# Kernel tuning notes

Hardware: AMD Instinct MI355X
Metric: run time of the kernel (lower is better)

## Reference

```python
import jax, jax.numpy as jnp
import numpy as np

B, S, L, D = 4, 8, 350, 768  # paragraphs, sentences/paragraph, padded pair length, hidden
P = B * S * (S - 1)          # number of ordered sentence pairs = 224

# pair p -> (z, j, k): same enumeration order as the torch nested loops
_IDX = np.array([(z, j, k) for z in range(B) for j in range(S) for k in range(S) if j != k])
# each pair contributes its first-sentence embedding to segment (z,j) and second to (z,k)
_SEG = np.stack([_IDX[:, 0] * S + _IDX[:, 1], _IDX[:, 0] * S + _IDX[:, 2]], axis=1).reshape(-1)  # [2P]


def setup_inputs() -> dict:
    key = jax.random.key(0)
    ks = jax.random.split(key, 8)
    sc = 0.02
    all_output = jax.random.normal(ks[0], (P, L, D), dtype=jnp.float32)
    first_sep = jax.random.randint(ks[1], (P,), 5, 150).astype(jnp.int32)           # > 1
    second_sep = (first_sep + jax.random.randint(ks[2], (P,), 5, 150)).astype(jnp.int32)  # > first_sep+1, < L
    W1 = jax.random.normal(ks[3], (D, D), dtype=jnp.float32) * sc
    b1 = jnp.zeros((D,), jnp.float32)
    v1 = jax.random.normal(ks[4], (D,), dtype=jnp.float32) * sc
    vb1 = jnp.zeros((), jnp.float32)
    W2 = jax.random.normal(ks[5], (D, D), dtype=jnp.float32) * sc
    b2 = jnp.zeros((D,), jnp.float32)
    v2 = jax.random.normal(ks[6], (D,), dtype=jnp.float32) * sc
    vb2 = jnp.zeros((), jnp.float32)
    return {"all_output": all_output, "first_sep": first_sep, "second_sep": second_sep,
            "W1": W1, "b1": b1, "v1": v1, "vb1": vb1,
            "W2": W2, "b2": b2, "v2": v2, "vb2": vb2}


def reference(all_output, first_sep, second_sep, W1, b1, v1, vb1, W2, b2, v2, vb2):
    # pair_embeddings = [CLS] token of every pair
    pair_embeddings = all_output[:, 0, :]  # [P, D]

    # ---- level one: masked attention pooling over word positions ----
    u = jnp.tanh(all_output @ W1 + b1)          # [P, L, D]
    scores = u @ v1 + vb1                       # [P, L]
    pos = jnp.arange(L)[None, :]                # [1, L]
    mask1 = (pos >= 1) & (pos < first_sep[:, None])                 # tokens 1..first_sep-1
    mask2 = (pos > first_sep[:, None]) & (pos < second_sep[:, None])  # first_sep+1..second_sep-1

    def pool(mask):
        s = jnp.where(mask, scores, -jnp.inf)
        w = jax.nn.softmax(s, axis=1)           # [P, L]
        return jnp.einsum('pl,pld->pd', w, all_output)

    e1 = pool(mask1)                            # [P, D] first-sentence embeddings
    e2 = pool(mask2)                            # [P, D] second-sentence embeddings
    emb = jnp.stack([e1, e2], axis=1).reshape(2 * P, D)  # [2P, D]

    # ---- level two: segment attention pooling per (paragraph, sentence) group ----
    seg = jnp.asarray(_SEG)                     # [2P] segment ids, num_segments = B*S
    u2 = jnp.tanh(emb @ W2 + b2)                # [2P, D]
    sc = u2 @ v2 + vb2                          # [2P]
    num_seg = B * S
    smax = jax.ops.segment_max(sc, seg, num_segments=num_seg)
    ex = jnp.exp(sc - smax[seg])
    denom = jax.ops.segment_sum(ex, seg, num_segments=num_seg)
    w = ex / denom[seg]                         # segment softmax weights
    out2 = jax.ops.segment_sum(w[:, None] * emb, seg, num_segments=num_seg).reshape(B, S, D)
    return (pair_embeddings, out2)
```

## Files before the change

kernel.cpp:

```cpp
#include <hip/hip_runtime.h>
#include <math.h>

#define LSEQ   350
#define DDIM   768
#define NPAIR  224
#define MROWS1 78400
#define NSLAB1 613

typedef short bf16x8 __attribute__((ext_vector_type(8)));
typedef float f32x4  __attribute__((ext_vector_type(4)));

typedef const unsigned int __attribute__((address_space(1)))* gas_ptr;
typedef unsigned int __attribute__((address_space(3)))* las_ptr;

__device__ __forceinline__ void gload_lds16(const void* g, void* l) {
  __builtin_amdgcn_global_load_lds((gas_ptr)g, (las_ptr)l, 16, 0, 0);
}

__device__ __forceinline__ unsigned short f2bf(float x) {
  unsigned int u = __float_as_uint(x);
  unsigned int r = (u + 0x7FFFu + ((u >> 16) & 1u)) >> 16;
  return (unsigned short)r;
}

__device__ __forceinline__ float tanh_fast(float x) {
  float e = __expf(2.f * x);
  return 1.f - 2.f / (e + 1.f);
}

__global__ __launch_bounds__(256) void k_w1t(const float* __restrict__ W,
                                             unsigned short* __restrict__ Wt) {
  __shared__ float tile[32][33];
  int bk = blockIdx.x * 32, bn = blockIdx.y * 32;
  int tx = threadIdx.x & 31, ty = threadIdx.x >> 5;
#pragma unroll
  for (int i = 0; i < 32; i += 8)
    tile[ty + i][tx] = W[(size_t)(bk + ty + i) * DDIM + bn + tx];
  __syncthreads();
#pragma unroll
  for (int i = 0; i < 32; i += 8)
    Wt[(size_t)(bn + ty + i) * DDIM + bk + tx] = f2bf(tile[tx][ty + i]);
}

__global__ __launch_bounds__(256) void k_conv(const float* __restrict__ X,
                                              const int* __restrict__ ssep,
                                              unsigned short* __restrict__ Xbf) {
  const int p = blockIdx.x, tile = blockIdx.y, z = blockIdx.z;
  if (tile * 128 >= ssep[p]) return;
  const int t = threadIdx.x;
  const size_t base4 = ((size_t)p * LSEQ + tile * 128 + z * 32) * (DDIM / 4);
  const size_t limit4 = (size_t)MROWS1 * (DDIM / 4);
  const float4* X4 = (const float4*)X;
  uint2* O2 = (uint2*)Xbf;
#pragma unroll
  for (int k = 0; k < 24; ++k) {
    size_t i4 = base4 + (size_t)k * 256 + t;
    if (i4 >= limit4) break;
    float4 x = X4[i4];
    unsigned int ux = __float_as_uint(x.x) + 0x8000u;
    unsigned int uy = __float_as_uint(x.y) + 0x8000u;
    unsigned int uz = __float_as_uint(x.z) + 0x8000u;
    unsigned int uw = __float_as_uint(x.w) + 0x8000u;
    O2[i4] = make_uint2(__builtin_amdgcn_perm(uy, ux, 0x07060302u),
                        __builtin_amdgcn_perm(uw, uz, 0x07060302u));
  }
}

__global__ __launch_bounds__(256, 4) void k_gemm_bf16(
    const unsigned short* __restrict__ Xbf, const unsigned short* __restrict__ Wt,
    const float* __restrict__ bias, const float* __restrict__ vv,
    const int* __restrict__ ssep, float* __restrict__ outs) {
  const int b = blockIdx.x;
  const int g = b / 48, r = b - g * 48;
  const int unit = g * 8 + (r & 7);
  const int nchunk = r >> 3;
  const int pair = unit / 3, tile = unit - pair * 3;
  if (tile * 128 >= ssep[pair]) return;

  const size_t arow0 = (size_t)pair * LSEQ + tile * 128;
  const int n0 = nchunk * 128;

  __shared__ unsigned short As[128 * 32];
  __shared__ unsigned short Bs[128 * 32];

  const int t = threadIdx.x;
  const int lane = t & 63, w = t >> 6;
  const int l15 = t & 15;
  const int quad = (t >> 4) & 3;
  const int wm = w >> 1, wn = w & 1;
  const int lrow = lane >> 2;
  const int lcol = (lane & 3) * 8;

  f32x4 acc[4][4];
#pragma unroll
  for (int mi = 0; mi < 4; ++mi)
#pragma unroll
    for (int ni = 0; ni < 4; ++ni)
#pragma unroll
      for (int q = 0; q < 4; ++q) acc[mi][ni][q] = 0.f;

  for (int k0 = 0; k0 < DDIM; k0 += 32) {
#pragma unroll
    for (int j = 0; j < 2; ++j) {
      int seg = w * 2 + j;
      gload_lds16(Xbf + (arow0 + seg * 16 + lrow) * DDIM + k0 + lcol, As + seg * 512);
      gload_lds16(Wt + (size_t)(n0 + seg * 16 + lrow) * DDIM + k0 + lcol, Bs + seg * 512);
    }
    __syncthreads();

    bf16x8 a[4], bfr[4];
#pragma unroll
    for (int mi = 0; mi < 4; ++mi)
      a[mi] = *(const bf16x8*)&As[(wm * 64 + mi * 16 + l15) * 32 + quad * 8];
#pragma unroll
    for (int ni = 0; ni < 4; ++ni)
      bfr[ni] = *(const bf16x8*)&Bs[(wn * 64 + ni * 16 + l15) * 32 + quad * 8];
#pragma unroll
    for (int mi = 0; mi < 4; ++mi)
#pragma unroll
      for (int ni = 0; ni < 4; ++ni)
        acc[mi][ni] = __builtin_amdgcn_mfma_f32_16x16x32_bf16(a[mi], bfr[ni], acc[mi][ni], 0, 0, 0);
    __syncthreads();
  }

  float vvv[4], bbv[4];
#pragma unroll
  for (int ni = 0; ni < 4; ++ni) {
    int n = n0 + wn * 64 + ni * 16 + l15;
    vvv[ni] = vv[n];
    bbv[ni] = bias[n];
  }
#pragma unroll
  for (int mi = 0; mi < 4; ++mi) {
#pragma unroll
    for (int reg = 0; reg < 4; ++reg) {
      float s = 0.f;
#pragma unroll
      for (int ni = 0; ni < 4; ++ni)
        s += tanh_fast(acc[mi][ni][reg] + bbv[ni]) * vvv[ni];
      s += __shfl_xor(s, 1);
      s += __shfl_xor(s, 2);
      s += __shfl_xor(s, 4);
      s += __shfl_xor(s, 8);
      if (l15 == mi * 4 + reg) {
        int l = tile * 128 + wm * 64 + mi * 16 + quad * 4 + reg;
        if (l < LSEQ) atomicAdd(&outs[pair * LSEQ + l], s);
      }
    }
  }
}

__global__ __launch_bounds__(256, 2) void k_gemm_score(
    const float* __restrict__ X, const unsigned short* __restrict__ Wt,
    const float* __restrict__ bias, const float* __restrict__ vv,
    float* __restrict__ outs, int Mrows, int swz) {
  int slab, nchunk;
  if (swz) {
    int b = blockIdx.x;
    int g = b / 48, r = b - g * 48;
    slab = g * 8 + (r & 7);
    nchunk = r >> 3;
    if (slab >= NSLAB1) return;
  } else {
    slab = blockIdx.y;
    nchunk = blockIdx.x;
  }
  const int row0 = slab * 128;
  const int n0 = nchunk * 128;

  __shared__ unsigned short As[128][40];
  __shared__ unsigned short Bs[128][40];

  const int t = threadIdx.x;
  const int l15 = t & 15;
  const int quad = (t >> 4) & 3;
  const int w = t >> 6;
  const int wm = w >> 1, wn = w & 1;
  const int ar = t >> 3;
  const int ac = (t & 7) * 4;
  const int br = t >> 2;
  const int bc = (t & 3) * 8;

  f32x4 acc[4][4];
#pragma unroll
  for (int mi = 0; mi < 4; ++mi)
#pragma unroll
    for (int ni = 0; ni < 4; ++ni)
#pragma unroll
      for (int q = 0; q < 4; ++q) acc[mi][ni][q] = 0.f;

  for (int k0 = 0; k0 < DDIM; k0 += 32) {
#pragma unroll
    for (int pass = 0; pass < 4; ++pass) {
      int rr = ar + pass * 32;
      int row = row0 + rr;
      float4 x = make_float4(0.f, 0.f, 0.f, 0.f);
      if (row < Mrows) x = *(const float4*)(X + (size_t)row * DDIM + k0 + ac);
      unsigned int ux = __float_as_uint(x.x) + 0x8000u;
      unsigned int uy = __float_as_uint(x.y) + 0x8000u;
      unsigned int uz = __float_as_uint(x.z) + 0x8000u;
      unsigned int uw = __float_as_uint(x.w) + 0x8000u;
      *(uint2*)&As[rr][ac] = make_uint2(__builtin_amdgcn_perm(uy, ux, 0x07060302u),
                                        __builtin_amdgcn_perm(uw, uz, 0x07060302u));
    }
#pragma unroll
    for (int pp = 0; pp < 2; ++pp) {
      int rr = br + pp * 64;
      *(uint4*)&Bs[rr][bc] = *(const uint4*)(Wt + (size_t)(n0 + rr) * DDIM + k0 + bc);
    }
    __syncthreads();

    bf16x8 a[4], bfr[4];
#pragma unroll
    for (int mi = 0; mi < 4; ++mi)
      a[mi] = *(const bf16x8*)&As[wm * 64 + mi * 16 + l15][quad * 8];
#pragma unroll
    for (int ni = 0; ni < 4; ++ni)
      bfr[ni] = *(const bf16x8*)&Bs[wn * 64 + ni * 16 + l15][quad * 8];
#pragma unroll
    for (int mi = 0; mi < 4; ++mi)
#pragma unroll
      for (int ni = 0; ni < 4; ++ni)
        acc[mi][ni] = __builtin_amdgcn_mfma_f32_16x16x32_bf16(a[mi], bfr[ni], acc[mi][ni], 0, 0, 0);
    __syncthreads();
  }

  float vvv[4], bbv[4];
#pragma unroll
  for (int ni = 0; ni < 4; ++ni) {
    int n = n0 + wn * 64 + ni * 16 + l15;
    vvv[ni] = vv[n];
    bbv[ni] = bias[n];
  }
#pragma unroll
  for (int mi = 0; mi < 4; ++mi) {
#pragma unroll
    for (int reg = 0; reg < 4; ++reg) {
      float s = 0.f;
#pragma unroll
      for (int ni = 0; ni < 4; ++ni)
        s += tanh_fast(acc[mi][ni][reg] + bbv[ni]) * vvv[ni];
      s += __shfl_xor(s, 1);
      s += __shfl_xor(s, 2);
      s += __shfl_xor(s, 4);
      s += __shfl_xor(s, 8);
      if (l15 == mi * 4 + reg) {
        int row = row0 + wm * 64 + mi * 16 + quad * 4 + reg;
        if (row < Mrows) atomicAdd(&outs[row], s);
      }
    }
  }
}

__device__ __forceinline__ float block_reduce(float v, bool is_max, float* redbuf) {
#pragma unroll
  for (int off = 1; off < 64; off <<= 1) {
    float o = __shfl_xor(v, off);
    v = is_max ? fmaxf(v, o) : (v + o);
  }
  int wv = threadIdx.x >> 6;
  if ((threadIdx.x & 63) == 0) redbuf[wv] = v;
  __syncthreads();
  float r = is_max ? fmaxf(fmaxf(redbuf[0], redbuf[1]), fmaxf(redbuf[2], redbuf[3]))
                   : (redbuf[0] + redbuf[1] + redbuf[2] + redbuf[3]);
  __syncthreads();
  return r;
}

__global__ __launch_bounds__(256) void k_smax(
    const float* __restrict__ scores, const int* __restrict__ fsep,
    const int* __restrict__ ssep, float* __restrict__ w1n, float* __restrict__ w2n) {
  const int p = blockIdx.x, t = threadIdx.x;
  const int fs = fsep[p], ss = ssep[p];
  __shared__ float redbuf[4];
  float s1a[2], s2a[2];
  float m1p = -INFINITY, m2p = -INFINITY;
#pragma unroll
  for (int i = 0; i < 2; ++i) {
    int l = t + i * 256;
    float s1 = -INFINITY, s2 = -INFINITY;
    if (l < LSEQ) {
      float s = scores[p * LSEQ + l];
      s1 = (l >= 1 && l < fs) ? s : -INFINITY;
      s2 = (l > fs && l < ss) ? s : -INFINITY;
    }
    s1a[i] = s1; s2a[i] = s2;
    m1p = fmaxf(m1p, s1); m2p = fmaxf(m2p, s2);
  }
  float m1 = block_reduce(m1p, true, redbuf);
  float m2 = block_reduce(m2p, true, redbuf);
  float d1p = 0.f, d2p = 0.f;
#pragma unroll
  for (int i = 0; i < 2; ++i) {
    s1a[i] = __expf(s1a[i] - m1);
    s2a[i] = __expf(s2a[i] - m2);
    d1p += s1a[i]; d2p += s2a[i];
  }
  float inv1 = 1.f / block_reduce(d1p, false, redbuf);
  float inv2 = 1.f / block_reduce(d2p, false, redbuf);
#pragma unroll
  for (int i = 0; i < 2; ++i) {
    int l = t + i * 256;
    if (l < LSEQ) {
      w1n[p * LSEQ + l] = s1a[i] * inv1;
      w2n[p * LSEQ + l] = s2a[i] * inv2;
    }
  }
}

__global__ __launch_bounds__(192) void k_pool_bf(
    const unsigned short* __restrict__ Xbf, const float* __restrict__ X,
    const float* __restrict__ w1n, const float* __restrict__ w2n,
    const int* __restrict__ ssep, float* __restrict__ emb, float* __restrict__ out) {
  const int p = blockIdx.x, c = blockIdx.y, t = threadIdx.x;
  const int ss = ssep[p];
  const size_t prow = (size_t)p * LSEQ;
  float A1[4] = {0.f, 0.f, 0.f, 0.f}, A2[4] = {0.f, 0.f, 0.f, 0.f};
  for (int l = 1 + c; l < ss; l += 8) {
    float wa = w1n[prow + l], wb = w2n[prow + l];
    uint2 xv = *(const uint2*)(Xbf + (prow + l) * DDIM + t * 4);
    float x0 = __uint_as_float((xv.x & 0xFFFFu) << 16);
    float x1 = __uint_as_float(xv.x & 0xFFFF0000u);
    float x2 = __uint_as_float((xv.y & 0xFFFFu) << 16);
    float x3 = __uint_as_float(xv.y & 0xFFFF0000u);
    A1[0] += wa * x0; A1[1] += wa * x1; A1[2] += wa * x2; A1[3] += wa * x3;
    A2[0] += wb * x0; A2[1] += wb * x1; A2[2] += wb * x2; A2[3] += wb * x3;
  }
  float* e1 = emb + (size_t)(2 * p) * DDIM + t * 4;
  float* e2 = emb + (size_t)(2 * p + 1) * DDIM + t * 4;
#pragma unroll
  for (int i = 0; i < 4; ++i) atomicAdd(&e1[i], A1[i]);
#pragma unroll
  for (int i = 0; i < 4; ++i) atomicAdd(&e2[i], A2[i]);
  if (c == 0) {
    *(float4*)(out + (size_t)p * DDIM + t * 4) = *(const float4*)(X + prow * DDIM + t * 4);
  }
}

__global__ __launch_bounds__(256) void k_pool(
    const float* __restrict__ X, const float* __restrict__ scores,
    const int* __restrict__ fsep, const int* __restrict__ ssep,
    float* __restrict__ emb, float* __restrict__ out) {
  const int p = blockIdx.x;
  const int c = blockIdx.y;
  const int t = threadIdx.x;
  const int fs = fsep[p], ss = ssep[p];
  __shared__ float sw1[LSEQ], sw2[LSEQ];
  __shared__ float redbuf[4];

  float m1p = -INFINITY, m2p = -INFINITY;
  for (int l = t; l < LSEQ; l += 256) {
    float s = scores[p * LSEQ + l];
    float s1 = (l >= 1 && l < fs) ? s : -INFINITY;
    float s2 = (l > fs && l < ss) ? s : -INFINITY;
    sw1[l] = s1; sw2[l] = s2;
    m1p = fmaxf(m1p, s1); m2p = fmaxf(m2p, s2);
  }
  __syncthreads();
  float m1 = block_reduce(m1p, true, redbuf);
  float m2 = block_reduce(m2p, true, redbuf);
  float d1p = 0.f, d2p = 0.f;
  for (int l = t; l < LSEQ; l += 256) {
    float e1v = __expf(sw1[l] - m1);
    float e2v = __expf(sw2[l] - m2);
    sw1[l] = e1v; sw2[l] = e2v;
    d1p += e1v; d2p += e2v;
  }
  __syncthreads();
  float inv1 = 1.f / block_reduce(d1p, false, redbuf);
  float inv2 = 1.f / block_reduce(d2p, false, redbuf);
  const float* base = X + (size_t)p * LSEQ * DDIM;
  if (c == 0) {
    float* po = out + (size_t)p * DDIM;
    po[t] = base[t]; po[t + 256] = base[t + 256]; po[t + 512] = base[t + 512];
  }
  if (t < 192) {
    float4 A1 = make_float4(0.f, 0.f, 0.f, 0.f);
    float4 A2 = make_float4(0.f, 0.f, 0.f, 0.f);
    for (int l = 1 + c; l < ss; l += 8) {
      float wa = sw1[l] * inv1, wb = sw2[l] * inv2;
      float4 x = *(const float4*)(base + (size_t)l * DDIM + 4 * t);
      A1.x += wa * x.x; A1.y += wa * x.y; A1.z += wa * x.z; A1.w += wa * x.w;
      A2.x += wb * x.x; A2.y += wb * x.y; A2.z += wb * x.z; A2.w += wb * x.w;
    }
    float* e1 = emb + (size_t)(2 * p) * DDIM + 4 * t;
    float* e2 = emb + (size_t)(2 * p + 1) * DDIM + 4 * t;
    atomicAdd(&e1[0], A1.x); atomicAdd(&e1[1], A1.y);
    atomicAdd(&e1[2], A1.z); atomicAdd(&e1[3], A1.w);
    atomicAdd(&e2[0], A2.x); atomicAdd(&e2[1], A2.y);
    atomicAdd(&e2[2], A2.z); atomicAdd(&e2[3], A2.w);
  }
}

__global__ __launch_bounds__(256) void k_segout(
    const float* __restrict__ emb, const float* __restrict__ sc,
    float* __restrict__ out2) {
  const int g = blockIdx.x;
  const int z = g >> 3, j = g & 7;
  const int t = threadIdx.x;
  int ee[14];
#pragma unroll
  for (int i = 0; i < 7; ++i) ee[i] = 2 * (z * 56 + j * 7 + i);
#pragma unroll
  for (int i = 0; i < 7; ++i) {
    int j2 = i + (i >= j ? 1 : 0);
    int kk = j - (j > j2 ? 1 : 0);
    ee[7 + i] = 2 * (z * 56 + j2 * 7 + kk) + 1;
  }
  float sv[14];
  float m = -INFINITY;
#pragma unroll
  for (int i = 0; i < 14; ++i) { sv[i] = sc[ee[i]]; m = fmaxf(m, sv[i]); }
  float den = 0.f;
#pragma unroll
  for (int i = 0; i < 14; ++i) { sv[i] = __expf(sv[i] - m); den += sv[i]; }
  float inv = 1.f / den;
  float a0 = 0.f, a1 = 0.f, a2 = 0.f;
#pragma unroll
  for (int i = 0; i < 14; ++i) {
    float wgt = sv[i] * inv;
    const float* er = emb + (size_t)ee[i] * DDIM;
    a0 += wgt * er[t]; a1 += wgt * er[t + 256]; a2 += wgt * er[t + 512];
  }
  out2[(size_t)g * DDIM + t] = a0;
  out2[(size_t)g * DDIM + t + 256] = a1;
  out2[(size_t)g * DDIM + t + 512] = a2;
}

extern "C" void kernel_launch(void* const* d_in, const int* in_sizes, int n_in,
                              void* d_out, int out_size, void* d_ws, size_t ws_size,
                              hipStream_t stream) {
  const float* X  = (const float*)d_in[0];
  const int* fs   = (const int*)d_in[1];
  const int* ss   = (const int*)d_in[2];
  const float* W1 = (const float*)d_in[3];
  const float* b1 = (const float*)d_in[4];
  const float* v1 = (const float*)d_in[5];
  const float* W2 = (const float*)d_in[7];
  const float* b2 = (const float*)d_in[8];
  const float* v2 = (const float*)d_in[9];
  float* out = (float*)d_out;

  char* ws = (char*)d_ws;
  const size_t XBF_BYTES = (size_t)78464 * DDIM * 2;
  const size_t OFF_WT  = XBF_BYTES;
  const size_t OFF_SC  = OFF_WT + 1179648;
  const size_t OFF_EMB = OFF_SC + 313600;
  const size_t OFF_W1N = OFF_EMB + 1376256;
  const size_t OFF_W2N = OFF_W1N + 313600;
  const size_t NEED    = OFF_W2N + 313600;

  if (ws_size >= NEED) {
    unsigned short* Xbf = (unsigned short*)ws;
    unsigned short* Wt  = (unsigned short*)(ws + OFF_WT);
    float* scores = (float*)(ws + OFF_SC);
    float* emb    = (float*)(ws + OFF_EMB);
    float* w1n    = (float*)(ws + OFF_W1N);
    float* w2n    = (float*)(ws + OFF_W2N);
    float* sc     = scores;

    k_w1t<<<dim3(24, 24), 256, 0, stream>>>(W1, Wt);
    hipMemsetAsync(scores, 0, MROWS1 * sizeof(float), stream);
    hipMemsetAsync(emb, 0, 448 * DDIM * sizeof(float), stream);
    k_conv<<<dim3(NPAIR, 3, 4), 256, 0, stream>>>(X, ss, Xbf);
    k_gemm_bf16<<<84 * 48, 256, 0, stream>>>(Xbf, Wt, b1, v1, ss, scores);
    k_smax<<<NPAIR, 256, 0, stream>>>(scores, fs, ss, w1n, w2n);
    k_pool_bf<<<dim3(NPAIR, 8), 192, 0, stream>>>(Xbf, X, w1n, w2n, ss, emb, out);
    k_w1t<<<dim3(24, 24), 256, 0, stream>>>(W2, Wt);
    hipMemsetAsync(sc, 0, 448 * sizeof(float), stream);
    k_gemm_score<<<dim3(6, 4), 256, 0, stream>>>(emb, Wt, b2, v2, sc, 448, 0);
    k_segout<<<32, 256, 0, stream>>>(emb, sc, out + (size_t)NPAIR * DDIM);
  } else {
    unsigned short* Wt = (unsigned short*)ws;
    float* scores = (float*)(ws + 1179648);
    float* emb    = (float*)(ws + 1493248);
    float* sc     = scores;

    k_w1t<<<dim3(24, 24), 256, 0, stream>>>(W1, Wt);
    hipMemsetAsync(scores, 0, MROWS1 * sizeof(float), stream);
    hipMemsetAsync(emb, 0, 448 * DDIM * sizeof(float), stream);
    k_gemm_score<<<77 * 48, 256, 0, stream>>>(X, Wt, b1, v1, scores, MROWS1, 1);
    k_pool<<<dim3(NPAIR, 8), 256, 0, stream>>>(X, scores, fs, ss, emb, out);
    k_w1t<<<dim3(24, 24), 256, 0, stream>>>(W2, Wt);
    hipMemsetAsync(sc, 0, 448 * sizeof(float), stream);
    k_gemm_score<<<dim3(6, 4), 256, 0, stream>>>(emb, Wt, b2, v2, sc, 448, 0);
    k_segout<<<32, 256, 0, stream>>>(emb, sc, out + (size_t)NPAIR * DDIM);
  }
}
```

Measured before the change: 546.7 us.

## Compact valid token rows across pairs before bf16 GEMM and fuse softmax into pooling

A prefix scan over second_sep computes per-pair row offsets. Only the valid rows 1..ss-1 are converted to bf16 into one contiguous buffer, with a rowmap back to the original positions. The level-one GEMM then tiles this compacted buffer in dense 128-row slabs, so it no longer wastes work on padded per-pair tiles. The softmax and pooling kernels are merged, both weight transposes run in one launch, and the memsets are combined. The cost is extra indirection and an atomic scatter through rowmap. The grid is fixed at 65*48 blocks, which assumes the compacted rows fit in 520 slabs.

```diff
diff --git a/kernel.cpp b/kernel.cpp
--- a/kernel.cpp
+++ b/kernel.cpp
@@ -6,6 +6,7 @@
 #define NPAIR  224
 #define MROWS1 78400
 #define NSLAB1 613
+#define MAXSLAB 520
 
 typedef short bf16x8 __attribute__((ext_vector_type(8)));
 typedef float f32x4  __attribute__((ext_vector_type(4)));
@@ -26,6 +27,42 @@
 __device__ __forceinline__ float tanh_fast(float x) {
   float e = __expf(2.f * x);
   return 1.f - 2.f / (e + 1.f);
+}
+
+__global__ __launch_bounds__(256) void k_scan(const int* __restrict__ ssep,
+                                              int* __restrict__ off) {
+  __shared__ int buf[256];
+  const int t = threadIdx.x;
+  int v = (t < NPAIR) ? (ssep[t] - 1) : 0;
+  buf[t] = v;
+  __syncthreads();
+#pragma unroll
+  for (int d = 1; d < 256; d <<= 1) {
+    int add = (t >= d) ? buf[t - d] : 0;
+    __syncthreads();
+    buf[t] += add;
+    __syncthreads();
+  }
+  if (t < NPAIR) off[t] = buf[t] - v;
+  if (t == NPAIR - 1) off[NPAIR] = buf[t];
+}
+
+__global__ __launch_bounds__(256) void k_wt2(const float* __restrict__ W1,
+                                             const float* __restrict__ W2,
+                                             unsigned short* __restrict__ Wt1,
+                                             unsigned short* __restrict__ Wt2) {
+  const float* W = blockIdx.z ? W2 : W1;
+  unsigned short* Wt = blockIdx.z ? Wt2 : Wt1;
+  __shared__ float tile[32][33];
+  int bk = blockIdx.x * 32, bn = blockIdx.y * 32;
+  int tx = threadIdx.x & 31, ty = threadIdx.x >> 5;
+#pragma unroll
+  for (int i = 0; i < 32; i += 8)
+    tile[ty + i][tx] = W[(size_t)(bk + ty + i) * DDIM + bn + tx];
+  __syncthreads();
+#pragma unroll
+  for (int i = 0; i < 32; i += 8)
+    Wt[(size_t)(bn + ty + i) * DDIM + bk + tx] = f2bf(tile[tx][ty + i]);
 }
 
 __global__ __launch_bounds__(256) void k_w1t(const float* __restrict__ W,
@@ -44,40 +81,47 @@
 
 __global__ __launch_bounds__(256) void k_conv(const float* __restrict__ X,
                                               const int* __restrict__ ssep,
-                                              unsigned short* __restrict__ Xbf) {
+                                              const int* __restrict__ off,
+                                              unsigned short* __restrict__ Xbf,
+                                              int* __restrict__ rowmap) {
   const int p = blockIdx.x, tile = blockIdx.y, z = blockIdx.z;
-  if (tile * 128 >= ssep[p]) return;
+  const int nrow = ssep[p] - 1;
+  const int r0 = tile * 128 + z * 32;
+  if (r0 >= nrow) return;
   const int t = threadIdx.x;
-  const size_t base4 = ((size_t)p * LSEQ + tile * 128 + z * 32) * (DDIM / 4);
-  const size_t limit4 = (size_t)MROWS1 * (DDIM / 4);
-  const float4* X4 = (const float4*)X;
-  uint2* O2 = (uint2*)Xbf;
-#pragma unroll
-  for (int k = 0; k < 24; ++k) {
-    size_t i4 = base4 + (size_t)k * 256 + t;
-    if (i4 >= limit4) break;
-    float4 x = X4[i4];
-    unsigned int ux = __float_as_uint(x.x) + 0x8000u;
-    unsigned int uy = __float_as_uint(x.y) + 0x8000u;
-    unsigned int uz = __float_as_uint(x.z) + 0x8000u;
-    unsigned int uw = __float_as_uint(x.w) + 0x8000u;
-    O2[i4] = make_uint2(__builtin_amdgcn_perm(uy, ux, 0x07060302u),
-                        __builtin_amdgcn_perm(uw, uz, 0x07060302u));
-  }
-}
-
-__global__ __launch_bounds__(256, 4) void k_gemm_bf16(
+  const int o = off[p];
+  if (t < 192) {
+    for (int i = 0; i < 32; ++i) {
+      int r = r0 + i;
+      if (r >= nrow) break;
+      float4 x = *(const float4*)(X + ((size_t)p * LSEQ + 1 + r) * DDIM + t * 4);
+      unsigned int ux = __float_as_uint(x.x) + 0x8000u;
+      unsigned int uy = __float_as_uint(x.y) + 0x8000u;
+      unsigned int uz = __float_as_uint(x.z) + 0x8000u;
+      unsigned int uw = __float_as_uint(x.w) + 0x8000u;
+      *(uint2*)(Xbf + (size_t)(o + r) * DDIM + t * 4) =
+          make_uint2(__builtin_amdgcn_perm(uy, ux, 0x07060302u),
+                     __builtin_amdgcn_perm(uw, uz, 0x07060302u));
+    }
+  } else if (t < 224) {
+    int r = r0 + (t - 192);
+    if (r < nrow) rowmap[o + r] = p * LSEQ + 1 + r;
+  }
+}
+
+__global__ __launch_bounds__(256, 4) void k_gemm_c(
     const unsigned short* __restrict__ Xbf, const unsigned short* __restrict__ Wt,
     const float* __restrict__ bias, const float* __restrict__ vv,
-    const int* __restrict__ ssep, float* __restrict__ outs) {
+    const int* __restrict__ off, const int* __restrict__ rowmap,
+    float* __restrict__ scores) {
+  const int Mtotal = off[NPAIR];
   const int b = blockIdx.x;
   const int g = b / 48, r = b - g * 48;
-  const int unit = g * 8 + (r & 7);
+  const int slab = g * 8 + (r & 7);
   const int nchunk = r >> 3;
-  const int pair = unit / 3, tile = unit - pair * 3;
-  if (tile * 128 >= ssep[pair]) return;
-
-  const size_t arow0 = (size_t)pair * LSEQ + tile * 128;
+  if (slab * 128 >= Mtotal) return;
+
+  const size_t arow0 = (size_t)slab * 128;
   const int n0 = nchunk * 128;
 
   __shared__ unsigned short As[128 * 32];
@@ -143,8 +187,8 @@
       s += __shfl_xor(s, 4);
       s += __shfl_xor(s, 8);
       if (l15 == mi * 4 + reg) {
-        int l = tile * 128 + wm * 64 + mi * 16 + quad * 4 + reg;
-        if (l < LSEQ) atomicAdd(&outs[pair * LSEQ + l], s);
+        int row = (int)arow0 + wm * 64 + mi * 16 + quad * 4 + reg;
+        if (row < Mtotal) atomicAdd(&scores[rowmap[row]], s);
       }
     }
   }
@@ -267,73 +311,62 @@
   return r;
 }
 
-__global__ __launch_bounds__(256) void k_smax(
+__global__ __launch_bounds__(256) void k_pool2(
+    const unsigned short* __restrict__ Xbf, const float* __restrict__ X,
     const float* __restrict__ scores, const int* __restrict__ fsep,
-    const int* __restrict__ ssep, float* __restrict__ w1n, float* __restrict__ w2n) {
-  const int p = blockIdx.x, t = threadIdx.x;
+    const int* __restrict__ ssep, const int* __restrict__ off,
+    float* __restrict__ emb, float* __restrict__ out) {
+  const int p = blockIdx.x, c = blockIdx.y, t = threadIdx.x;
   const int fs = fsep[p], ss = ssep[p];
+  __shared__ float sw1[LSEQ], sw2[LSEQ];
   __shared__ float redbuf[4];
-  float s1a[2], s2a[2];
+
   float m1p = -INFINITY, m2p = -INFINITY;
-#pragma unroll
-  for (int i = 0; i < 2; ++i) {
-    int l = t + i * 256;
-    float s1 = -INFINITY, s2 = -INFINITY;
-    if (l < LSEQ) {
-      float s = scores[p * LSEQ + l];
-      s1 = (l >= 1 && l < fs) ? s : -INFINITY;
-      s2 = (l > fs && l < ss) ? s : -INFINITY;
-    }
-    s1a[i] = s1; s2a[i] = s2;
+  for (int l = t; l < LSEQ; l += 256) {
+    float s = scores[p * LSEQ + l];
+    float s1 = (l >= 1 && l < fs) ? s : -INFINITY;
+    float s2 = (l > fs && l < ss) ? s : -INFINITY;
+    sw1[l] = s1; sw2[l] = s2;
     m1p = fmaxf(m1p, s1); m2p = fmaxf(m2p, s2);
   }
+  __syncthreads();
   float m1 = block_reduce(m1p, true, redbuf);
   float m2 = block_reduce(m2p, true, redbuf);
   float d1p = 0.f, d2p = 0.f;
-#pragma unroll
-  for (int i = 0; i < 2; ++i) {
-    s1a[i] = __expf(s1a[i] - m1);
-    s2a[i] = __expf(s2a[i] - m2);
-    d1p += s1a[i]; d2p += s2a[i];
-  }
+  for (int l = t; l < LSEQ; l += 256) {
+    float e1v = __expf(sw1[l] - m1);
+    float e2v = __expf(sw2[l] - m2);
+    sw1[l] = e1v; sw2[l] = e2v;
+    d1p += e1v; d2p += e2v;
+  }
+  __syncthreads();
   float inv1 = 1.f / block_reduce(d1p, false, redbuf);
   float inv2 = 1.f / block_reduce(d2p, false, redbuf);
-#pragma unroll
-  for (int i = 0; i < 2; ++i) {
-    int l = t + i * 256;
-    if (l < LSEQ) {
-      w1n[p * LSEQ + l] = s1a[i] * inv1;
-      w2n[p * LSEQ + l] = s2a[i] * inv2;
-    }
-  }
-}
-
-__global__ __launch_bounds__(192) void k_pool_bf(
-    const unsigned short* __restrict__ Xbf, const float* __restrict__ X,
-    const float* __restrict__ w1n, const float* __restrict__ w2n,
-    const int* __restrict__ ssep, float* __restrict__ emb, float* __restrict__ out) {
-  const int p = blockIdx.x, c = blockIdx.y, t = threadIdx.x;
-  const int ss = ssep[p];
-  const size_t prow = (size_t)p * LSEQ;
-  float A1[4] = {0.f, 0.f, 0.f, 0.f}, A2[4] = {0.f, 0.f, 0.f, 0.f};
-  for (int l = 1 + c; l < ss; l += 8) {
-    float wa = w1n[prow + l], wb = w2n[prow + l];
-    uint2 xv = *(const uint2*)(Xbf + (prow + l) * DDIM + t * 4);
-    float x0 = __uint_as_float((xv.x & 0xFFFFu) << 16);
-    float x1 = __uint_as_float(xv.x & 0xFFFF0000u);
-    float x2 = __uint_as_float((xv.y & 0xFFFFu) << 16);
-    float x3 = __uint_as_float(xv.y & 0xFFFF0000u);
-    A1[0] += wa * x0; A1[1] += wa * x1; A1[2] += wa * x2; A1[3] += wa * x3;
-    A2[0] += wb * x0; A2[1] += wb * x1; A2[2] += wb * x2; A2[3] += wb * x3;
-  }
-  float* e1 = emb + (size_t)(2 * p) * DDIM + t * 4;
-  float* e2 = emb + (size_t)(2 * p + 1) * DDIM + t * 4;
-#pragma unroll
-  for (int i = 0; i < 4; ++i) atomicAdd(&e1[i], A1[i]);
-#pragma unroll
-  for (int i = 0; i < 4; ++i) atomicAdd(&e2[i], A2[i]);
-  if (c == 0) {
-    *(float4*)(out + (size_t)p * DDIM + t * 4) = *(const float4*)(X + prow * DDIM + t * 4);
+
+  if (c == 0 && t < 192) {
+    *(float4*)(out + (size_t)p * DDIM + t * 4) =
+        *(const float4*)(X + (size_t)p * LSEQ * DDIM + t * 4);
+  }
+
+  if (t < 192) {
+    const int o = off[p];
+    float A1[4] = {0.f, 0.f, 0.f, 0.f}, A2[4] = {0.f, 0.f, 0.f, 0.f};
+    for (int l = 1 + c; l < ss; l += 8) {
+      float wa = sw1[l] * inv1, wb = sw2[l] * inv2;
+      uint2 xv = *(const uint2*)(Xbf + (size_t)(o + l - 1) * DDIM + t * 4);
+      float x0 = __uint_as_float((xv.x & 0xFFFFu) << 16);
+      float x1 = __uint_as_float(xv.x & 0xFFFF0000u);
+      float x2 = __uint_as_float((xv.y & 0xFFFFu) << 16);
+      float x3 = __uint_as_float(xv.y & 0xFFFF0000u);
+      A1[0] += wa * x0; A1[1] += wa * x1; A1[2] += wa * x2; A1[3] += wa * x3;
+      A2[0] += wb * x0; A2[1] += wb * x1; A2[2] += wb * x2; A2[3] += wb * x3;
+    }
+    float* e1 = emb + (size_t)(2 * p) * DDIM + t * 4;
+    float* e2 = emb + (size_t)(2 * p + 1) * DDIM + t * 4;
+#pragma unroll
+    for (int i = 0; i < 4; ++i) atomicAdd(&e1[i], A1[i]);
+#pragma unroll
+    for (int i = 0; i < 4; ++i) atomicAdd(&e2[i], A2[i]);
   }
 }
 
@@ -442,33 +475,33 @@
   float* out = (float*)d_out;
 
   char* ws = (char*)d_ws;
-  const size_t XBF_BYTES = (size_t)78464 * DDIM * 2;
-  const size_t OFF_WT  = XBF_BYTES;
-  const size_t OFF_SC  = OFF_WT + 1179648;
-  const size_t OFF_EMB = OFF_SC + 313600;
-  const size_t OFF_W1N = OFF_EMB + 1376256;
-  const size_t OFF_W2N = OFF_W1N + 313600;
-  const size_t NEED    = OFF_W2N + 313600;
+  const size_t XBF_ROWS = (size_t)MAXSLAB * 128 + 64;
+  const size_t OFF_MAP  = XBF_ROWS * DDIM * 2;
+  const size_t OFF_OFF  = OFF_MAP + XBF_ROWS * 4;
+  const size_t OFF_WT1  = OFF_OFF + 1024;
+  const size_t OFF_WT2  = OFF_WT1 + 1179648;
+  const size_t OFF_SCORES = OFF_WT2 + 1179648;
+  const size_t OFF_EMB  = OFF_SCORES + 313600;
+  const size_t OFF_SC   = OFF_EMB + 1376256;
+  const size_t NEED     = OFF_SC + 2048;
 
   if (ws_size >= NEED) {
     unsigned short* Xbf = (unsigned short*)ws;
-    unsigned short* Wt  = (unsigned short*)(ws + OFF_WT);
-    float* scores = (float*)(ws + OFF_SC);
+    int*   rowmap = (int*)(ws + OFF_MAP);
+    int*   off    = (int*)(ws + OFF_OFF);
+    unsigned short* Wt1 = (unsigned short*)(ws + OFF_WT1);
+    unsigned short* Wt2 = (unsigned short*)(ws + OFF_WT2);
+    float* scores = (float*)(ws + OFF_SCORES);
     float* emb    = (float*)(ws + OFF_EMB);
-    float* w1n    = (float*)(ws + OFF_W1N);
-    float* w2n    = (float*)(ws + OFF_W2N);
-    float* sc     = scores;
-
-    k_w1t<<<dim3(24, 24), 256, 0, stream>>>(W1, Wt);
-    hipMemsetAsync(scores, 0, MROWS1 * sizeof(float), stream);
-    hipMemsetAsync(emb, 0, 448 * DDIM * sizeof(float), stream);
-    k_conv<<<dim3(NPAIR, 3, 4), 256, 0, stream>>>(X, ss, Xbf);
-    k_gemm_bf16<<<84 * 48, 256, 0, stream>>>(Xbf, Wt, b1, v1, ss, scores);
-    k_smax<<<NPAIR, 256, 0, stream>>>(scores, fs, ss, w1n, w2n);
-    k_pool_bf<<<dim3(NPAIR, 8), 192, 0, stream>>>(Xbf, X, w1n, w2n, ss, emb, out);
-    k_w1t<<<dim3(24, 24), 256, 0, stream>>>(W2, Wt);
-    hipMemsetAsync(sc, 0, 448 * sizeof(float), stream);
-    k_gemm_score<<<dim3(6, 4), 256, 0, stream>>>(emb, Wt, b2, v2, sc, 448, 0);
+    float* sc     = (float*)(ws + OFF_SC);
+
+    k_scan<<<1, 256, 0, stream>>>(ss, off);
+    k_wt2<<<dim3(24, 24, 2), 256, 0, stream>>>(W1, W2, Wt1, Wt2);
+    hipMemsetAsync(scores, 0, 313600 + 1376256 + 2048, stream);
+    k_conv<<<dim3(NPAIR, 3, 4), 256, 0, stream>>>(X, ss, off, Xbf, rowmap);
+    k_gemm_c<<<65 * 48, 256, 0, stream>>>(Xbf, Wt1, b1, v1, off, rowmap, scores);
+    k_pool2<<<dim3(NPAIR, 8), 256, 0, stream>>>(Xbf, X, scores, fs, ss, off, emb, out);
+    k_gemm_score<<<dim3(6, 4), 256, 0, stream>>>(emb, Wt2, b2, v2, sc, 448, 0);
     k_segout<<<32, 256, 0, stream>>>(emb, sc, out + (size_t)NPAIR * DDIM);
   } else {
     unsigned short* Wt = (unsigned short*)ws;
```

Result: faster. 500.0 us (-8.5%).
